# Kernel tuning notes

Measured on AMD Instinct MI355X. Metric: run time of the kernel, lower is better.

The kernel has to match this reference:

```python
import jax, jax.numpy as jnp
import numpy as np

N_NODES = 50000
N_EDGES = 100000
IN_FEATS = 32
EDGE_FEATS = 32
HIDDEN = 32
OUT = 3


def setup_inputs() -> dict:
    key = jax.random.key(0)
    ks = jax.random.split(key, 16)
    s = 0.05
    return {
        "node_feats": jax.random.normal(ks[0], (N_NODES, IN_FEATS), jnp.float32),
        "edge_feats": jax.random.normal(ks[1], (N_EDGES, EDGE_FEATS), jnp.float32),
        "src": jax.random.randint(ks[2], (N_EDGES,), 0, N_NODES, jnp.int32),
        "dst": jax.random.randint(ks[3], (N_EDGES,), 0, N_NODES, jnp.int32),
        "edge_indices": jnp.arange(N_EDGES, dtype=jnp.int32),
        # edge_network: Linear(edge_feats, hidden*in) -> ReLU -> Linear(hidden*in, hidden*in)
        "W1": jax.random.normal(ks[4], (EDGE_FEATS, HIDDEN * IN_FEATS), jnp.float32) * s,
        "b1": jax.random.normal(ks[5], (HIDDEN * IN_FEATS,), jnp.float32) * s,
        "W2": jax.random.normal(ks[6], (HIDDEN * IN_FEATS, HIDDEN * IN_FEATS), jnp.float32) * s,
        "b2": jax.random.normal(ks[7], (HIDDEN * IN_FEATS,), jnp.float32) * s,
        # NNConv bias
        "conv_bias": jax.random.normal(ks[8], (HIDDEN,), jnp.float32) * s,
        # edge classifier: Linear(2*hidden+edge_feats, hidden) -> ReLU -> Linear(hidden, out)
        "Wc1": jax.random.normal(ks[9], (2 * HIDDEN + EDGE_FEATS, HIDDEN), jnp.float32) * s,
        "bc1": jax.random.normal(ks[10], (HIDDEN,), jnp.float32) * s,
        "Wc2": jax.random.normal(ks[11], (HIDDEN, OUT), jnp.float32) * s,
        "bc2": jax.random.normal(ks[12], (OUT,), jnp.float32) * s,
    }


def reference(node_feats, edge_feats, src, dst, edge_indices,
              W1, b1, W2, b2, conv_bias, Wc1, bc1, Wc2, bc2):
    N = node_feats.shape[0]
    E = edge_feats.shape[0]
    in_f = node_feats.shape[1]
    hid = conv_bias.shape[0]

    # edge-conditioned weights: MLP(efeat) -> [E, in, hidden]
    w = jax.nn.relu(edge_feats @ W1 + b1) @ W2 + b2
    w = w.reshape(E, in_f, hid)

    # per-edge matmul of gathered src features, then mean-aggregate into dst (DGL NNConv, aggregator='mean')
    msg = jnp.einsum("ei,eio->eo", node_feats[src], w)  # [E, hidden]
    agg = jax.ops.segment_sum(msg, dst, num_segments=N)  # [N, hidden]
    deg = jax.ops.segment_sum(jnp.ones((E,), msg.dtype), dst, num_segments=N)
    agg = agg / jnp.maximum(deg, 1.0)[:, None]
    h = jax.nn.relu(agg + conv_bias)  # [N, hidden]

    # gather-concat-MLP edge classifier
    s = src[edge_indices]
    d = dst[edge_indices]
    edge_in = jnp.concatenate([h[s], h[d], edge_feats[edge_indices]], axis=1)
    logits = jax.nn.relu(edge_in @ Wc1 + bc1) @ Wc2 + bc2
    return logits
```

## Files before the change

### kernel.cpp

```cpp
#include <hip/hip_runtime.h>
#include <hip/hip_bf16.h>
#include <stdint.h>

#define NNODES 50000
#define NEDGES 100000

typedef __attribute__((ext_vector_type(8))) short short8;
typedef __attribute__((ext_vector_type(4))) float f32x4;

__device__ __forceinline__ unsigned short f2bf(float f) {
    union { unsigned int i; float f; } v; v.f = f;
    unsigned int r = v.i + 0x7FFFu + ((v.i >> 16) & 1u);
    return (unsigned short)(r >> 16);
}
__device__ __forceinline__ void gload16(const void* g, void* lds) {
    __builtin_amdgcn_global_load_lds(
        (const __attribute__((address_space(1))) unsigned int*)g,
        (__attribute__((address_space(3))) unsigned int*)lds, 16, 0, 0);
}

__global__ __launch_bounds__(256) void k_pack(const float* __restrict__ W2,
                                              unsigned short* __restrict__ w2p) {
    const int idx = blockIdx.x * 256 + threadIdx.x;
    const int k = idx >> 10, col = idx & 1023;
    const float v = W2[idx];
    const int nb = col >> 7, n = col & 127;
    const int ks = k >> 5, kg = (k >> 3) & 3, j = k & 7;
    w2p[((((size_t)nb * 32 + ks) * 4 + kg) * 128 + n) * 8 + j] = f2bf(v);
}

__global__ __launch_bounds__(256) void k_packw1(const float* __restrict__ W1,
                                                unsigned short* __restrict__ w1pT) {
    const int idx = blockIdx.x * 256 + threadIdx.x;
    const int i = idx >> 10, col = idx & 1023;
    const float v = W1[idx];
    const int ks = col >> 5, c = col & 31;
    const int kt = c >> 4, lr = c & 15;
    const int lq = i >> 3, ii = i & 7;
    w1pT[((((size_t)ks * 2 + kt) * 4 + lq) * 16 + lr) * 8 + ii] = f2bf(v);
}

__global__ __launch_bounds__(256, 2) void k_gemm(
    const unsigned short* __restrict__ w2p, const unsigned short* __restrict__ w1pT,
    const float* __restrict__ ef, const float* __restrict__ nf,
    const float* __restrict__ b1, const float* __restrict__ b2,
    const int* __restrict__ src, const int* __restrict__ dst,
    float* __restrict__ agg, float* __restrict__ deg)
{
    __shared__ __align__(16) unsigned short sE[4096];
    __shared__ __align__(16) unsigned short sXb[4096];
    __shared__ __align__(16) unsigned short sH[4096];
    __shared__ __align__(16) unsigned short sB[2][8192];
    __shared__ float sX[128 * 36];
    __shared__ int   sD[128];

    const int t    = threadIdx.x;
    const int lane = t & 63;
    const int w    = t >> 6;
    const int lq   = lane >> 4, lr = lane & 15;
    const int e0   = blockIdx.x * 128;

    {
        const int e = t >> 1, fo = (t & 1) * 16;
        const int eg = e0 + e;
        const bool valid = eg < NEDGES;
        const int iq = fo >> 3;

        float4 v[4];
        #pragma unroll
        for (int q = 0; q < 4; ++q)
            v[q] = valid ? *(const float4*)(ef + (size_t)eg * 32 + fo + q * 4)
                         : float4{0.f, 0.f, 0.f, 0.f};
        unsigned short hh[16];
        #pragma unroll
        for (int q = 0; q < 4; ++q) {
            hh[q*4+0] = f2bf(v[q].x); hh[q*4+1] = f2bf(v[q].y);
            hh[q*4+2] = f2bf(v[q].z); hh[q*4+3] = f2bf(v[q].w);
        }
        uint4 pa, pb;
        pa.x = hh[0] | ((unsigned)hh[1] << 16);  pa.y = hh[2]  | ((unsigned)hh[3] << 16);
        pa.z = hh[4] | ((unsigned)hh[5] << 16);  pa.w = hh[6]  | ((unsigned)hh[7] << 16);
        pb.x = hh[8] | ((unsigned)hh[9] << 16);  pb.y = hh[10] | ((unsigned)hh[11] << 16);
        pb.z = hh[12]| ((unsigned)hh[13] << 16); pb.w = hh[14] | ((unsigned)hh[15] << 16);
        *(uint4*)(sE + ((iq    ) * 128 + e) * 8) = pa;
        *(uint4*)(sE + ((iq + 1) * 128 + e) * 8) = pb;

        const int s = valid ? src[eg] : 0;
        #pragma unroll
        for (int q = 0; q < 4; ++q) {
            float4 xv = valid ? *(const float4*)(nf + (size_t)s * 32 + fo + q * 4)
                              : float4{0.f, 0.f, 0.f, 0.f};
            *(float4*)(sX + e * 36 + fo + q * 4) = xv;
            hh[q*4+0] = f2bf(xv.x); hh[q*4+1] = f2bf(xv.y);
            hh[q*4+2] = f2bf(xv.z); hh[q*4+3] = f2bf(xv.w);
        }
        pa.x = hh[0] | ((unsigned)hh[1] << 16);  pa.y = hh[2]  | ((unsigned)hh[3] << 16);
        pa.z = hh[4] | ((unsigned)hh[5] << 16);  pa.w = hh[6]  | ((unsigned)hh[7] << 16);
        pb.x = hh[8] | ((unsigned)hh[9] << 16);  pb.y = hh[10] | ((unsigned)hh[11] << 16);
        pb.z = hh[12]| ((unsigned)hh[13] << 16); pb.w = hh[14] | ((unsigned)hh[15] << 16);
        *(uint4*)(sXb + ((iq    ) * 128 + e) * 8) = pa;
        *(uint4*)(sXb + ((iq + 1) * 128 + e) * 8) = pb;
    }
    if (t < 128) {
        const int eg = e0 + t;
        const int dv = (eg < NEDGES) ? dst[eg] : -1;
        sD[t] = dv;
        if (dv >= 0) atomicAdd(&deg[dv], 1.0f);
    }
    __syncthreads();

    const short8 bfe0 = *(const short8*)(sE + (lq * 128 + w * 32      + lr) * 8);
    const short8 bfe1 = *(const short8*)(sE + (lq * 128 + w * 32 + 16 + lr) * 8);

    f32x4 pm4[4];
    {
        const short8 xf0 = *(const short8*)(sXb + (lq * 128 + w * 32      + lr) * 8);
        const short8 xf1 = *(const short8*)(sXb + (lq * 128 + w * 32 + 16 + lr) * 8);
        short8 bb0, bb1;
        #pragma unroll
        for (int j = 0; j < 8; ++j) {
            bb0[j] = (short)f2bf(b2[(lq * 8 + j) * 32 + lr]);
            bb1[j] = (short)f2bf(b2[(lq * 8 + j) * 32 + 16 + lr]);
        }
        const f32x4 z = {0.f, 0.f, 0.f, 0.f};
        pm4[0] = __builtin_amdgcn_mfma_f32_16x16x32_bf16(xf0, bb0, z, 0, 0, 0);
        pm4[1] = __builtin_amdgcn_mfma_f32_16x16x32_bf16(xf0, bb1, z, 0, 0, 0);
        pm4[2] = __builtin_amdgcn_mfma_f32_16x16x32_bf16(xf1, bb0, z, 0, 0, 0);
        pm4[3] = __builtin_amdgcn_mfma_f32_16x16x32_bf16(xf1, bb1, z, 0, 0, 0);
    }

    #define STAGE2(dstb, nblk_, ks_) do {                                          \
        const unsigned short* _g0 = w2p + ((size_t)((nblk_) * 32 + (ks_)) * 4096); \
        const unsigned short* _g1 = _g0 + (size_t)32 * 4096;                       \
        gload16(_g0 + (size_t)t * 8,         (dstb) + w * 512);                    \
        gload16(_g0 + (size_t)(t + 256) * 8, (dstb) + 2048 + w * 512);             \
        gload16(_g1 + (size_t)t * 8,         (dstb) + 4096 + w * 512);             \
        gload16(_g1 + (size_t)(t + 256) * 8, (dstb) + 6144 + w * 512);             \
    } while (0)

    int buf = 0;
    STAGE2(sB[0], 0, 0);

    short8 w1c0 = *(const short8*)(w1pT + ((0 * 4 + lq) * 16 + lr) * 8);
    short8 w1c1 = *(const short8*)(w1pT + ((1 * 4 + lq) * 16 + lr) * 8);
    float4 b1c0 = *(const float4*)(b1 + lq * 4);
    float4 b1c1 = *(const float4*)(b1 + 16 + lq * 4);

    for (int nbp = 0; nbp < 4; ++nbp) {
        const int nblk0 = nbp * 2;
        f32x4 acc[2][16];
        #pragma unroll
        for (int mt = 0; mt < 2; ++mt)
            #pragma unroll
            for (int nt = 0; nt < 16; ++nt) acc[mt][nt] = f32x4{0.f, 0.f, 0.f, 0.f};

        for (int ks = 0; ks < 32; ++ks) {
            __syncthreads();
            {
                int nks = ks + 1, nnb = nblk0;
                if (nks == 32) { nks = 0; nnb = nblk0 + 2; }
                if (!(nbp == 3 && ks == 31)) STAGE2(sB[buf ^ 1], nnb, nks);
            }
            const int nks2 = (ks == 31) ? 0 : ks + 1;
            short8 w1n0 = *(const short8*)(w1pT + ((((size_t)nks2 * 2 + 0) * 4 + lq) * 16 + lr) * 8);
            short8 w1n1 = *(const short8*)(w1pT + ((((size_t)nks2 * 2 + 1) * 4 + lq) * 16 + lr) * 8);
            float4 b1n0 = *(const float4*)(b1 + nks2 * 32      + lq * 4);
            float4 b1n1 = *(const float4*)(b1 + nks2 * 32 + 16 + lq * 4);

            f32x4 h00 = {b1c0.x, b1c0.y, b1c0.z, b1c0.w};
            f32x4 h01 = h00;
            f32x4 h10 = {b1c1.x, b1c1.y, b1c1.z, b1c1.w};
            f32x4 h11 = h10;
            h00 = __builtin_amdgcn_mfma_f32_16x16x32_bf16(w1c0, bfe0, h00, 0, 0, 0);
            h01 = __builtin_amdgcn_mfma_f32_16x16x32_bf16(w1c0, bfe1, h01, 0, 0, 0);
            h10 = __builtin_amdgcn_mfma_f32_16x16x32_bf16(w1c1, bfe0, h10, 0, 0, 0);
            h11 = __builtin_amdgcn_mfma_f32_16x16x32_bf16(w1c1, bfe1, h11, 0, 0, 0);

            #define STORE_H1(hv, kt, et) do {                                          \
                float r0 = fmaxf((hv)[0], 0.f), r1 = fmaxf((hv)[1], 0.f);              \
                float r2 = fmaxf((hv)[2], 0.f), r3 = fmaxf((hv)[3], 0.f);              \
                unsigned p0, p1;                                                        \
                asm("v_cvt_pk_bf16_f32 %0, %1, %2" : "=v"(p0) : "v"(r0), "v"(r1));      \
                asm("v_cvt_pk_bf16_f32 %0, %1, %2" : "=v"(p1) : "v"(r2), "v"(r3));      \
                uint2 pk; pk.x = p0; pk.y = p1;                                         \
                *(uint2*)(sH + w * 1024 +                                               \
                    (((kt) * 2 + (lq >> 1)) * 32 + (et) * 16 + lr) * 8 + (lq & 1) * 4)  \
                    = pk;                                                               \
            } while (0)
            STORE_H1(h00, 0, 0); STORE_H1(h01, 0, 1);
            STORE_H1(h10, 1, 0); STORE_H1(h11, 1, 1);
            #undef STORE_H1

            const unsigned short* pa = sH + w * 1024;
            const short8 af0 = *(const short8*)(pa + (lq * 32      + lr) * 8);
            const short8 af1 = *(const short8*)(pa + (lq * 32 + 16 + lr) * 8);
            const unsigned short* pb = sB[buf];
            #pragma unroll
            for (int np = 0; np < 2; ++np)
                #pragma unroll
                for (int nt = 0; nt < 8; ++nt) {
                    const short8 bf = *(const short8*)(pb + np * 4096 + (lq * 128 + nt * 16 + lr) * 8);
                    acc[0][np*8+nt] = __builtin_amdgcn_mfma_f32_16x16x32_bf16(af0, bf, acc[0][np*8+nt], 0, 0, 0);
                    acc[1][np*8+nt] = __builtin_amdgcn_mfma_f32_16x16x32_bf16(af1, bf, acc[1][np*8+nt], 0, 0, 0);
                }
            buf ^= 1;
            w1c0 = w1n0; w1c1 = w1n1; b1c0 = b1n0; b1c1 = b1n1;
        }

        #pragma unroll
        for (int np = 0; np < 2; ++np) {
            const int nblk = nblk0 + np;
            #pragma unroll
            for (int nt = 0; nt < 8; ++nt) {
                const int i    = nblk * 4 + (nt >> 1);
                const int half = nt & 1;
                #pragma unroll
                for (int mt = 0; mt < 2; ++mt)
                    #pragma unroll
                    for (int r = 0; r < 4; ++r) {
                        const float x = sX[(w * 32 + mt * 16 + lq * 4 + r) * 36 + i];
                        pm4[mt * 2 + half][r] = fmaf(x, acc[mt][np*8+nt][r], pm4[mt * 2 + half][r]);
                    }
            }
        }
    }
    #undef STAGE2

    #pragma unroll
    for (int mt = 0; mt < 2; ++mt)
        #pragma unroll
        for (int r = 0; r < 4; ++r) {
            const int el = w * 32 + mt * 16 + lq * 4 + r;
            const int d  = sD[el];
            if (d >= 0) {
                atomicAdd(agg + (size_t)d * 32 + lr,      pm4[mt * 2][r]);
                atomicAdd(agg + (size_t)d * 32 + 16 + lr, pm4[mt * 2 + 1][r]);
            }
        }
}

__global__ __launch_bounds__(256) void k_node(
    float* __restrict__ agg, const float* __restrict__ deg,
    const float* __restrict__ cbias)
{
    const int idx = blockIdx.x * 256 + threadIdx.x;
    if (idx >= NNODES * 32) return;
    const int n = idx >> 5, o = idx & 31;
    const float d = fmaxf(deg[n], 1.0f);
    agg[idx] = fmaxf(agg[idx] / d + cbias[o], 0.0f);
}

__global__ __launch_bounds__(256) void k_cls(
    const float* __restrict__ h, const float* __restrict__ ef,
    const int* __restrict__ src, const int* __restrict__ dst,
    const int* __restrict__ eidx,
    const float* __restrict__ Wc1, const float* __restrict__ bc1,
    const float* __restrict__ Wc2, const float* __restrict__ bc2,
    float* __restrict__ out)
{
    __shared__ float s_w1[96 * 32];
    __shared__ float s_w2[96];
    __shared__ float s_b1[32];
    __shared__ float s_in[8][96];

    const int t = threadIdx.x;
    #pragma unroll
    for (int q = 0; q < 3; ++q)
        *(float4*)&s_w1[t * 12 + q * 4] = *(const float4*)&Wc1[t * 12 + q * 4];
    if (t < 96) s_w2[t] = Wc2[t];
    if (t >= 96 && t < 128) s_b1[t - 96] = bc1[t - 96];

    const int ee = t >> 5, l = t & 31;
    const int e  = blockIdx.x * 8 + ee;
    const int ei = eidx[e];
    const int s = src[ei], d = dst[ei];
    s_in[ee][l]      = h[(size_t)s * 32 + l];
    s_in[ee][32 + l] = h[(size_t)d * 32 + l];
    s_in[ee][64 + l] = ef[(size_t)ei * 32 + l];
    __syncthreads();

    float acc = s_b1[l];
    #pragma unroll
    for (int c = 0; c < 96; ++c) acc = fmaf(s_in[ee][c], s_w1[c * 32 + l], acc);
    acc = fmaxf(acc, 0.f);

    float p0 = acc * s_w2[l * 3 + 0];
    float p1 = acc * s_w2[l * 3 + 1];
    float p2 = acc * s_w2[l * 3 + 2];
    #pragma unroll
    for (int m = 1; m <= 16; m <<= 1) {
        p0 += __shfl_xor(p0, m);
        p1 += __shfl_xor(p1, m);
        p2 += __shfl_xor(p2, m);
    }
    if (l == 0) {
        out[(size_t)e * 3 + 0] = p0 + bc2[0];
        out[(size_t)e * 3 + 1] = p1 + bc2[1];
        out[(size_t)e * 3 + 2] = p2 + bc2[2];
    }
}

extern "C" void kernel_launch(void* const* d_in, const int* in_sizes, int n_in,
                              void* d_out, int out_size, void* d_ws, size_t ws_size,
                              hipStream_t stream) {
    const float* nf   = (const float*)d_in[0];
    const float* ef   = (const float*)d_in[1];
    const int*   src  = (const int*)d_in[2];
    const int*   dst  = (const int*)d_in[3];
    const int*   eidx = (const int*)d_in[4];
    const float* W1   = (const float*)d_in[5];
    const float* b1   = (const float*)d_in[6];
    const float* W2   = (const float*)d_in[7];
    const float* b2   = (const float*)d_in[8];
    const float* cb   = (const float*)d_in[9];
    const float* Wc1  = (const float*)d_in[10];
    const float* bc1  = (const float*)d_in[11];
    const float* Wc2  = (const float*)d_in[12];
    const float* bc2  = (const float*)d_in[13];
    float* out = (float*)d_out;

    float* agg = (float*)d_ws;
    float* deg = agg + (size_t)NNODES * 32;
    unsigned short* w2p  = (unsigned short*)(deg + NNODES);
    unsigned short* w1pT = w2p + 1048576;

    hipMemsetAsync(d_ws, 0, ((size_t)NNODES * 32 + NNODES) * 4, stream);
    k_pack<<<4096, 256, 0, stream>>>(W2, w2p);
    k_packw1<<<128, 256, 0, stream>>>(W1, w1pT);

    k_gemm<<<(NEDGES + 127) / 128, 256, 0, stream>>>(
        w2p, w1pT, ef, nf, b1, b2, src, dst, agg, deg);

    k_node<<<(NNODES * 32 + 255) / 256, 256, 0, stream>>>(agg, deg, cb);
    k_cls<<<NEDGES / 8, 256, 0, stream>>>(agg, ef, src, dst, eidx, Wc1, bc1, Wc2, bc2, out);
}
```

Baseline: 354.9 us.

## Retile edge GEMM to 2x2 wave grid sharing B tiles and shrink LDS

Changes the wave decomposition of the fused edge-MLP GEMM from four waves each covering 32 edges across 256 columns to a 2x2 grid: each wave covers 64 edges across 128 columns. Each B fragment read from LDS now feeds four MFMAs instead of two, and the first-layer activations go into one shared sH tile. The fp32 sX buffer is dropped in favour of the bf16 copy, and sE is aliased onto the B buffer, which cuts LDS use and may allow higher occupancy. The two column-half waves are combined through an LDS reduction before the atomic adds to agg. The cost is extra block-wide barriers per k-step and bf16 precision for the x multiplier.

```diff
diff --git a/kernel.cpp b/kernel.cpp
--- a/kernel.cpp
+++ b/kernel.cpp
@@ -12,6 +12,9 @@
     union { unsigned int i; float f; } v; v.f = f;
     unsigned int r = v.i + 0x7FFFu + ((v.i >> 16) & 1u);
     return (unsigned short)(r >> 16);
+}
+__device__ __forceinline__ float bf2f(unsigned short u) {
+    union { unsigned int i; float f; } v; v.i = ((unsigned int)u) << 16; return v.f;
 }
 __device__ __forceinline__ void gload16(const void* g, void* lds) {
     __builtin_amdgcn_global_load_lds(
@@ -47,37 +50,35 @@
     const int* __restrict__ src, const int* __restrict__ dst,
     float* __restrict__ agg, float* __restrict__ deg)
 {
-    __shared__ __align__(16) unsigned short sE[4096];
+    __shared__ __align__(16) unsigned short sB[2][8192];
+    __shared__ __align__(16) unsigned short sH[4096];
     __shared__ __align__(16) unsigned short sXb[4096];
-    __shared__ __align__(16) unsigned short sH[4096];
-    __shared__ __align__(16) unsigned short sB[2][8192];
-    __shared__ float sX[128 * 36];
-    __shared__ int   sD[128];
+    __shared__ int sD[128];
 
     const int t    = threadIdx.x;
     const int lane = t & 63;
     const int w    = t >> 6;
+    const int wm   = w >> 1, wc = w & 1;
     const int lq   = lane >> 4, lr = lane & 15;
     const int e0   = blockIdx.x * 128;
+
+    unsigned short* sE = sB[0];
 
     {
         const int e = t >> 1, fo = (t & 1) * 16;
         const int eg = e0 + e;
         const bool valid = eg < NEDGES;
         const int iq = fo >> 3;
-
-        float4 v[4];
-        #pragma unroll
-        for (int q = 0; q < 4; ++q)
-            v[q] = valid ? *(const float4*)(ef + (size_t)eg * 32 + fo + q * 4)
-                         : float4{0.f, 0.f, 0.f, 0.f};
         unsigned short hh[16];
+        uint4 pa, pb;
+
         #pragma unroll
         for (int q = 0; q < 4; ++q) {
-            hh[q*4+0] = f2bf(v[q].x); hh[q*4+1] = f2bf(v[q].y);
-            hh[q*4+2] = f2bf(v[q].z); hh[q*4+3] = f2bf(v[q].w);
-        }
-        uint4 pa, pb;
+            float4 v = valid ? *(const float4*)(ef + (size_t)eg * 32 + fo + q * 4)
+                             : float4{0.f, 0.f, 0.f, 0.f};
+            hh[q*4+0] = f2bf(v.x); hh[q*4+1] = f2bf(v.y);
+            hh[q*4+2] = f2bf(v.z); hh[q*4+3] = f2bf(v.w);
+        }
         pa.x = hh[0] | ((unsigned)hh[1] << 16);  pa.y = hh[2]  | ((unsigned)hh[3] << 16);
         pa.z = hh[4] | ((unsigned)hh[5] << 16);  pa.w = hh[6]  | ((unsigned)hh[7] << 16);
         pb.x = hh[8] | ((unsigned)hh[9] << 16);  pb.y = hh[10] | ((unsigned)hh[11] << 16);
@@ -90,7 +91,6 @@
         for (int q = 0; q < 4; ++q) {
             float4 xv = valid ? *(const float4*)(nf + (size_t)s * 32 + fo + q * 4)
                               : float4{0.f, 0.f, 0.f, 0.f};
-            *(float4*)(sX + e * 36 + fo + q * 4) = xv;
             hh[q*4+0] = f2bf(xv.x); hh[q*4+1] = f2bf(xv.y);
             hh[q*4+2] = f2bf(xv.z); hh[q*4+3] = f2bf(xv.w);
         }
@@ -109,25 +109,27 @@
     }
     __syncthreads();
 
-    const short8 bfe0 = *(const short8*)(sE + (lq * 128 + w * 32      + lr) * 8);
+    const short8 bfe0 = *(const short8*)(sE + (lq * 128 + w * 32 + lr) * 8);
     const short8 bfe1 = *(const short8*)(sE + (lq * 128 + w * 32 + 16 + lr) * 8);
 
-    f32x4 pm4[4];
-    {
-        const short8 xf0 = *(const short8*)(sXb + (lq * 128 + w * 32      + lr) * 8);
-        const short8 xf1 = *(const short8*)(sXb + (lq * 128 + w * 32 + 16 + lr) * 8);
+    f32x4 pm[8];
+    #pragma unroll
+    for (int i = 0; i < 8; ++i) pm[i] = f32x4{0.f, 0.f, 0.f, 0.f};
+    if (wc == 0) {
         short8 bb0, bb1;
         #pragma unroll
         for (int j = 0; j < 8; ++j) {
             bb0[j] = (short)f2bf(b2[(lq * 8 + j) * 32 + lr]);
             bb1[j] = (short)f2bf(b2[(lq * 8 + j) * 32 + 16 + lr]);
         }
-        const f32x4 z = {0.f, 0.f, 0.f, 0.f};
-        pm4[0] = __builtin_amdgcn_mfma_f32_16x16x32_bf16(xf0, bb0, z, 0, 0, 0);
-        pm4[1] = __builtin_amdgcn_mfma_f32_16x16x32_bf16(xf0, bb1, z, 0, 0, 0);
-        pm4[2] = __builtin_amdgcn_mfma_f32_16x16x32_bf16(xf1, bb0, z, 0, 0, 0);
-        pm4[3] = __builtin_amdgcn_mfma_f32_16x16x32_bf16(xf1, bb1, z, 0, 0, 0);
-    }
+        #pragma unroll
+        for (int mt = 0; mt < 4; ++mt) {
+            const short8 xf = *(const short8*)(sXb + (lq * 128 + wm * 64 + mt * 16 + lr) * 8);
+            pm[mt * 2]     = __builtin_amdgcn_mfma_f32_16x16x32_bf16(xf, bb0, pm[mt * 2],     0, 0, 0);
+            pm[mt * 2 + 1] = __builtin_amdgcn_mfma_f32_16x16x32_bf16(xf, bb1, pm[mt * 2 + 1], 0, 0, 0);
+        }
+    }
+    __syncthreads();
 
     #define STAGE2(dstb, nblk_, ks_) do {                                          \
         const unsigned short* _g0 = w2p + ((size_t)((nblk_) * 32 + (ks_)) * 4096); \
@@ -138,7 +140,6 @@
         gload16(_g1 + (size_t)(t + 256) * 8, (dstb) + 6144 + w * 512);             \
     } while (0)
 
-    int buf = 0;
     STAGE2(sB[0], 0, 0);
 
     short8 w1c0 = *(const short8*)(w1pT + ((0 * 4 + lq) * 16 + lr) * 8);
@@ -146,27 +147,16 @@
     float4 b1c0 = *(const float4*)(b1 + lq * 4);
     float4 b1c1 = *(const float4*)(b1 + 16 + lq * 4);
 
+    int buf = 0;
     for (int nbp = 0; nbp < 4; ++nbp) {
         const int nblk0 = nbp * 2;
-        f32x4 acc[2][16];
-        #pragma unroll
-        for (int mt = 0; mt < 2; ++mt)
-            #pragma unroll
-            for (int nt = 0; nt < 16; ++nt) acc[mt][nt] = f32x4{0.f, 0.f, 0.f, 0.f};
+        f32x4 acc[4][8];
+        #pragma unroll
+        for (int mt = 0; mt < 4; ++mt)
+            #pragma unroll
+            for (int nt = 0; nt < 8; ++nt) acc[mt][nt] = f32x4{0.f, 0.f, 0.f, 0.f};
 
         for (int ks = 0; ks < 32; ++ks) {
-            __syncthreads();
-            {
-                int nks = ks + 1, nnb = nblk0;
-                if (nks == 32) { nks = 0; nnb = nblk0 + 2; }
-                if (!(nbp == 3 && ks == 31)) STAGE2(sB[buf ^ 1], nnb, nks);
-            }
-            const int nks2 = (ks == 31) ? 0 : ks + 1;
-            short8 w1n0 = *(const short8*)(w1pT + ((((size_t)nks2 * 2 + 0) * 4 + lq) * 16 + lr) * 8);
-            short8 w1n1 = *(const short8*)(w1pT + ((((size_t)nks2 * 2 + 1) * 4 + lq) * 16 + lr) * 8);
-            float4 b1n0 = *(const float4*)(b1 + nks2 * 32      + lq * 4);
-            float4 b1n1 = *(const float4*)(b1 + nks2 * 32 + 16 + lq * 4);
-
             f32x4 h00 = {b1c0.x, b1c0.y, b1c0.z, b1c0.w};
             f32x4 h01 = h00;
             f32x4 h10 = {b1c1.x, b1c1.y, b1c1.z, b1c1.w};
@@ -176,67 +166,105 @@
             h10 = __builtin_amdgcn_mfma_f32_16x16x32_bf16(w1c1, bfe0, h10, 0, 0, 0);
             h11 = __builtin_amdgcn_mfma_f32_16x16x32_bf16(w1c1, bfe1, h11, 0, 0, 0);
 
-            #define STORE_H1(hv, kt, et) do {                                          \
-                float r0 = fmaxf((hv)[0], 0.f), r1 = fmaxf((hv)[1], 0.f);              \
-                float r2 = fmaxf((hv)[2], 0.f), r3 = fmaxf((hv)[3], 0.f);              \
-                unsigned p0, p1;                                                        \
-                asm("v_cvt_pk_bf16_f32 %0, %1, %2" : "=v"(p0) : "v"(r0), "v"(r1));      \
-                asm("v_cvt_pk_bf16_f32 %0, %1, %2" : "=v"(p1) : "v"(r2), "v"(r3));      \
-                uint2 pk; pk.x = p0; pk.y = p1;                                         \
-                *(uint2*)(sH + w * 1024 +                                               \
-                    (((kt) * 2 + (lq >> 1)) * 32 + (et) * 16 + lr) * 8 + (lq & 1) * 4)  \
-                    = pk;                                                               \
+            __syncthreads();
+
+            #define STORE_H1(hv, kt, et) do {                                           \
+                float r0 = fmaxf((hv)[0], 0.f), r1 = fmaxf((hv)[1], 0.f);               \
+                float r2 = fmaxf((hv)[2], 0.f), r3 = fmaxf((hv)[3], 0.f);               \
+                unsigned p0, p1;                                                         \
+                asm("v_cvt_pk_bf16_f32 %0, %1, %2" : "=v"(p0) : "v"(r0), "v"(r1));       \
+                asm("v_cvt_pk_bf16_f32 %0, %1, %2" : "=v"(p1) : "v"(r2), "v"(r3));       \
+                uint2 pk; pk.x = p0; pk.y = p1;                                          \
+                *(uint2*)(sH + ((((kt) * 2 + (lq >> 1)) * 128 + w * 32 + (et) * 16 + lr) \
+                    * 8 + (lq & 1) * 4)) = pk;                                           \
             } while (0)
             STORE_H1(h00, 0, 0); STORE_H1(h01, 0, 1);
             STORE_H1(h10, 1, 0); STORE_H1(h11, 1, 1);
             #undef STORE_H1
 
-            const unsigned short* pa = sH + w * 1024;
-            const short8 af0 = *(const short8*)(pa + (lq * 32      + lr) * 8);
-            const short8 af1 = *(const short8*)(pa + (lq * 32 + 16 + lr) * 8);
-            const unsigned short* pb = sB[buf];
-            #pragma unroll
-            for (int np = 0; np < 2; ++np)
-                #pragma unroll
-                for (int nt = 0; nt < 8; ++nt) {
-                    const short8 bf = *(const short8*)(pb + np * 4096 + (lq * 128 + nt * 16 + lr) * 8);
-                    acc[0][np*8+nt] = __builtin_amdgcn_mfma_f32_16x16x32_bf16(af0, bf, acc[0][np*8+nt], 0, 0, 0);
-                    acc[1][np*8+nt] = __builtin_amdgcn_mfma_f32_16x16x32_bf16(af1, bf, acc[1][np*8+nt], 0, 0, 0);
-                }
+            __syncthreads();
+
+            {
+                int nks = ks + 1, nnb = nblk0;
+                if (nks == 32) { nks = 0; nnb = nblk0 + 2; }
+                if (!(nbp == 3 && ks == 31)) STAGE2(sB[buf ^ 1], nnb, nks);
+            }
+            const int nks2 = (ks == 31) ? 0 : ks + 1;
+            short8 w1n0 = *(const short8*)(w1pT + ((((size_t)nks2 * 2 + 0) * 4 + lq) * 16 + lr) * 8);
+            short8 w1n1 = *(const short8*)(w1pT + ((((size_t)nks2 * 2 + 1) * 4 + lq) * 16 + lr) * 8);
+            float4 b1n0 = *(const float4*)(b1 + nks2 * 32 + lq * 4);
+            float4 b1n1 = *(const float4*)(b1 + nks2 * 32 + 16 + lq * 4);
+
+            const short8 af0 = *(const short8*)(sH + (lq * 128 + wm * 64 +  0 + lr) * 8);
+            const short8 af1 = *(const short8*)(sH + (lq * 128 + wm * 64 + 16 + lr) * 8);
+            const short8 af2 = *(const short8*)(sH + (lq * 128 + wm * 64 + 32 + lr) * 8);
+            const short8 af3 = *(const short8*)(sH + (lq * 128 + wm * 64 + 48 + lr) * 8);
+            const unsigned short* pb = sB[buf] + wc * 4096;
+            #pragma unroll
+            for (int nt = 0; nt < 8; ++nt) {
+                const short8 bf = *(const short8*)(pb + (lq * 128 + nt * 16 + lr) * 8);
+                acc[0][nt] = __builtin_amdgcn_mfma_f32_16x16x32_bf16(af0, bf, acc[0][nt], 0, 0, 0);
+                acc[1][nt] = __builtin_amdgcn_mfma_f32_16x16x32_bf16(af1, bf, acc[1][nt], 0, 0, 0);
+                acc[2][nt] = __builtin_amdgcn_mfma_f32_16x16x32_bf16(af2, bf, acc[2][nt], 0, 0, 0);
+                acc[3][nt] = __builtin_amdgcn_mfma_f32_16x16x32_bf16(af3, bf, acc[3][nt], 0, 0, 0);
+            }
             buf ^= 1;
             w1c0 = w1n0; w1c1 = w1n1; b1c0 = b1n0; b1c1 = b1n1;
         }
 
-        #pragma unroll
-        for (int np = 0; np < 2; ++np) {
-            const int nblk = nblk0 + np;
-            #pragma unroll
-            for (int nt = 0; nt < 8; ++nt) {
-                const int i    = nblk * 4 + (nt >> 1);
-                const int half = nt & 1;
+        {
+            const int nblk = nblk0 + wc;
+            #pragma unroll
+            for (int ii = 0; ii < 4; ++ii) {
+                const int i  = nblk * 4 + ii;
+                const int iq = i >> 3, io = i & 7;
                 #pragma unroll
-                for (int mt = 0; mt < 2; ++mt)
+                for (int mt = 0; mt < 4; ++mt)
                     #pragma unroll
                     for (int r = 0; r < 4; ++r) {
-                        const float x = sX[(w * 32 + mt * 16 + lq * 4 + r) * 36 + i];
-                        pm4[mt * 2 + half][r] = fmaf(x, acc[mt][np*8+nt][r], pm4[mt * 2 + half][r]);
+                        const int e = wm * 64 + mt * 16 + lq * 4 + r;
+                        const float x = bf2f(sXb[iq * 1024 + e * 8 + io]);
+                        pm[mt*2+0][r] = fmaf(x, acc[mt][ii*2+0][r], pm[mt*2+0][r]);
+                        pm[mt*2+1][r] = fmaf(x, acc[mt][ii*2+1][r], pm[mt*2+1][r]);
                     }
             }
         }
     }
     #undef STAGE2
 
-    #pragma unroll
-    for (int mt = 0; mt < 2; ++mt)
-        #pragma unroll
-        for (int r = 0; r < 4; ++r) {
-            const int el = w * 32 + mt * 16 + lq * 4 + r;
-            const int d  = sD[el];
-            if (d >= 0) {
-                atomicAdd(agg + (size_t)d * 32 + lr,      pm4[mt * 2][r]);
-                atomicAdd(agg + (size_t)d * 32 + 16 + lr, pm4[mt * 2 + 1][r]);
-            }
-        }
+    __syncthreads();
+    float* sRed = (float*)sB;
+    if (wc == 0) {
+        #pragma unroll
+        for (int mt = 0; mt < 4; ++mt)
+            #pragma unroll
+            for (int r = 0; r < 4; ++r) {
+                const int e = wm * 64 + mt * 16 + lq * 4 + r;
+                sRed[e * 36 + lr]      = pm[mt*2][r];
+                sRed[e * 36 + 16 + lr] = pm[mt*2+1][r];
+            }
+    }
+    __syncthreads();
+    if (wc == 1) {
+        #pragma unroll
+        for (int mt = 0; mt < 4; ++mt)
+            #pragma unroll
+            for (int r = 0; r < 4; ++r) {
+                const int e = wm * 64 + mt * 16 + lq * 4 + r;
+                sRed[e * 36 + lr]      += pm[mt*2][r];
+                sRed[e * 36 + 16 + lr] += pm[mt*2+1][r];
+            }
+    }
+    __syncthreads();
+    {
+        const int e = t >> 1, o0 = (t & 1) * 16;
+        const int d = sD[e];
+        if (d >= 0) {
+            float* ap = agg + (size_t)d * 32 + o0;
+            #pragma unroll
+            for (int o = 0; o < 16; ++o) atomicAdd(ap + o, sRed[e * 36 + o0 + o]);
+        }
+    }
 }
 
 __global__ __launch_bounds__(256) void k_node(
```

New measurement: 486.0 us. 36.9% more time.
